# Performance work log

Measured on AMD Instinct MI355X. Metric: run time of the kernel, lower is better.

Reference implementation:

```python
import jax, jax.numpy as jnp
import numpy as np

ATT_HEAD, IN_DIM, OUT_DIM = 8, 768, 96
B, N = 8, 1024
LEAKY_ALPHA = 0.2


def setup_inputs() -> dict:
    key = jax.random.key(0)
    ks = jax.random.split(key, 8)
    feat_in = jax.random.normal(ks[0], (B, N, IN_DIM), dtype=jnp.float32)
    adj = jax.random.randint(ks[1], (B, N, N), 0, 2).astype(jnp.float32)
    # xavier-ish init scales
    W = jax.random.normal(ks[2], (ATT_HEAD, IN_DIM, OUT_DIM), dtype=jnp.float32) * (1.0 / np.sqrt(IN_DIM))
    b = jnp.zeros((OUT_DIM,), dtype=jnp.float32)
    w_src = jax.random.normal(ks[3], (ATT_HEAD, OUT_DIM, 1), dtype=jnp.float32) * (1.0 / np.sqrt(OUT_DIM))
    w_dst = jax.random.normal(ks[4], (ATT_HEAD, OUT_DIM, 1), dtype=jnp.float32) * (1.0 / np.sqrt(OUT_DIM))
    Hw = jax.random.normal(ks[5], (IN_DIM, IN_DIM), dtype=jnp.float32) * (1.0 / np.sqrt(IN_DIM))
    Hb = jnp.zeros((IN_DIM,), dtype=jnp.float32)
    return {"feat_in": feat_in, "adj": adj, "W": W, "b": b,
            "w_src": w_src, "w_dst": w_dst, "Hw": Hw, "Hb": Hb}


def reference(feat_in, adj, W, b, w_src, w_dst, Hw, Hb):
    batch, n, _ = feat_in.shape
    # per-head projection: [B,H,N,O]
    h = jnp.einsum('bni,hio->bhno', feat_in, W)
    t = jnp.tanh(h)
    a_src = jnp.einsum('bhno,hoq->bhnq', t, w_src)[..., 0]  # [B,H,N]
    a_dst = jnp.einsum('bhno,hoq->bhnq', t, w_dst)[..., 0]  # [B,H,N]
    attn = a_src[:, :, :, None] + a_dst[:, :, None, :]       # [B,H,N,N]
    attn = jnp.where(attn >= 0, attn, LEAKY_ALPHA * attn)
    mask = adj[:, None, :, :] == 0                            # 1-adj as bool
    attn = jnp.where(mask, jnp.float32(-999.0), attn)
    attn = jax.nn.softmax(attn, axis=-1)
    feat_out = jnp.einsum('bhnm,bhmo->bhno', attn, h) + b     # [B,H,N,O]
    feat_out = jnp.transpose(feat_out, (0, 2, 1, 3)).reshape(batch, n, -1)
    feat_out = jax.nn.elu(feat_out)
    gate = jax.nn.sigmoid(feat_in @ Hw.T + Hb)
    return gate * feat_out + (1.0 - gate) * feat_in
```

## Files before the change

### kernel.cpp

```cpp
#include <hip/hip_runtime.h>
#include <cstddef>

#define BATCH 8
#define NN 1024
#define IN_DIM 768
#define OUT_DIM 96
#define HEADS 8
#define M_ROWS 8192
#define NCOLS 1536

typedef __attribute__((ext_vector_type(8))) short short8;
typedef __attribute__((ext_vector_type(4))) float f32x4;
typedef __attribute__((ext_vector_type(4))) unsigned short ushort4v;

__device__ __forceinline__ unsigned short f2bf(float x) {
    unsigned int u = __builtin_bit_cast(unsigned int, x);
    u += 0x7fffu + ((u >> 16) & 1u);
    return (unsigned short)(u >> 16);
}
__device__ __forceinline__ float bf2f(unsigned short u) {
    unsigned int v = ((unsigned int)u) << 16;
    return __builtin_bit_cast(float, v);
}
__device__ __forceinline__ float tanh_fast(float x) {
    return 1.f - 2.f / (__expf(2.f * x) + 1.f);
}

__global__ void xb_kernel(const float* __restrict__ x, unsigned short* __restrict__ xb) {
    int idx = blockIdx.x * 256 + threadIdx.x;
    const float4* p = (const float4*)(x + (size_t)idx * 8);
    float4 a = p[0], b = p[1];
    short8 r;
    r[0] = (short)f2bf(a.x); r[1] = (short)f2bf(a.y); r[2] = (short)f2bf(a.z); r[3] = (short)f2bf(a.w);
    r[4] = (short)f2bf(b.x); r[5] = (short)f2bf(b.y); r[6] = (short)f2bf(b.z); r[7] = (short)f2bf(b.w);
    *(short8*)(xb + (size_t)idx * 8) = r;
}

__global__ void pack_w_kernel(const float* __restrict__ W, unsigned short* __restrict__ BT) {
    int idx = blockIdx.x * 256 + threadIdx.x;
    int c = idx / IN_DIM, i = idx % IN_DIM;
    int h = c / OUT_DIM, o = c % OUT_DIM;
    BT[(size_t)c * IN_DIM + i] = f2bf(W[((size_t)h * IN_DIM + i) * OUT_DIM + o]);
}
__global__ void pack_hw_kernel(const float* __restrict__ Hw, unsigned short* __restrict__ BT) {
    int idx = blockIdx.x * 256 + threadIdx.x;
    int c = idx / IN_DIM, i = idx % IN_DIM;
    BT[(size_t)(768 + c) * IN_DIM + i] = f2bf(Hw[(size_t)c * IN_DIM + i]);
}

__global__ void pack_abits_kernel(const float* __restrict__ adj, unsigned int* __restrict__ abits) {
    int idx = blockIdx.x * 256 + threadIdx.x;
    const float4* p = (const float4*)(adj + (size_t)idx * 32);
    unsigned int m = 0;
    #pragma unroll
    for (int q = 0; q < 8; ++q) {
        float4 v = p[q];
        m |= (v.x != 0.f ? 1u : 0u) << (q * 4 + 0);
        m |= (v.y != 0.f ? 1u : 0u) << (q * 4 + 1);
        m |= (v.z != 0.f ? 1u : 0u) << (q * 4 + 2);
        m |= (v.w != 0.f ? 1u : 0u) << (q * 4 + 3);
    }
    abits[idx] = m;
}

__global__ __launch_bounds__(256) void gemm1_kernel(
        const unsigned short* __restrict__ Xb, const unsigned short* __restrict__ BT,
        unsigned short* __restrict__ h_bt, float* __restrict__ glog) {
    __shared__ unsigned short As[128 * 72];
    __shared__ unsigned short Bs[128 * 72];
    int m0 = blockIdx.x * 128;
    int c0 = blockIdx.y * 128;
    int t = threadIdx.x;
    int w = t >> 6, lane = t & 63, l15 = t & 15, quad = lane >> 4;
    f32x4 acc[2][8] = {};
    for (int k0 = 0; k0 < IN_DIM; k0 += 64) {
        __syncthreads();
        #pragma unroll
        for (int q = 0; q < 4; ++q) {
            int f = t + q * 256;
            int r = f >> 3, c8 = (f & 7) * 8;
            *(short8*)(As + r * 72 + c8) = *(const short8*)(Xb + (size_t)(m0 + r) * IN_DIM + k0 + c8);
            *(short8*)(Bs + r * 72 + c8) = *(const short8*)(BT + (size_t)(c0 + r) * IN_DIM + k0 + c8);
        }
        __syncthreads();
        #pragma unroll
        for (int ks = 0; ks < 2; ++ks) {
            short8 af[2], bfr[8];
            #pragma unroll
            for (int mt = 0; mt < 2; ++mt)
                af[mt] = *(const short8*)(As + (w * 32 + mt * 16 + l15) * 72 + ks * 32 + quad * 8);
            #pragma unroll
            for (int nt = 0; nt < 8; ++nt)
                bfr[nt] = *(const short8*)(Bs + (nt * 16 + l15) * 72 + ks * 32 + quad * 8);
            #pragma unroll
            for (int mt = 0; mt < 2; ++mt)
                #pragma unroll
                for (int nt = 0; nt < 8; ++nt)
                    acc[mt][nt] = __builtin_amdgcn_mfma_f32_16x16x32_bf16(af[mt], bfr[nt], acc[mt][nt], 0, 0, 0);
        }
    }
    int b = m0 >> 10;
    #pragma unroll
    for (int mt = 0; mt < 2; ++mt) {
        int rowbase = m0 + w * 32 + mt * 16 + quad * 4;
        int nbase = rowbase & 1023;
        #pragma unroll
        for (int nt = 0; nt < 8; ++nt) {
            int c = c0 + nt * 16 + l15;
            if (c < 768) {
                int hh = c / OUT_DIM, o = c % OUT_DIM;
                ushort4v hb;
                hb[0] = f2bf(acc[mt][nt][0]); hb[1] = f2bf(acc[mt][nt][1]);
                hb[2] = f2bf(acc[mt][nt][2]); hb[3] = f2bf(acc[mt][nt][3]);
                *(ushort4v*)(h_bt + ((size_t)(b * 8 + hh) * OUT_DIM + o) * NN + nbase) = hb;
            } else {
                int cg = c - 768;
                #pragma unroll
                for (int reg = 0; reg < 4; ++reg)
                    glog[(size_t)(rowbase + reg) * 768 + cg] = acc[mt][nt][reg];
            }
        }
    }
}

__global__ __launch_bounds__(256) void a_kernel(const unsigned short* __restrict__ h_bt,
                                                const float* __restrict__ w_src,
                                                const float* __restrict__ w_dst,
                                                float* __restrict__ a_src, float* __restrict__ a_dst) {
    __shared__ unsigned short ht[96 * 72];
    __shared__ float ws_s[96], wd_s[96];
    __shared__ float pps[4][64], ppd[4][64];
    int bh = blockIdx.x >> 4;
    int n0 = (blockIdx.x & 15) * 64;
    int head = bh & 7;
    int t = threadIdx.x;
    if (t < 96) { ws_s[t] = w_src[head * 96 + t]; wd_s[t] = w_dst[head * 96 + t]; }
    for (int f = t; f < 768; f += 256) {
        int row = f >> 3, c8 = (f & 7) * 8;
        *(short8*)(ht + row * 72 + c8) = *(const short8*)(h_bt + ((size_t)bh * 96 + row) * NN + n0 + c8);
    }
    __syncthreads();
    int n = t & 63, part = t >> 6;
    float ps = 0.f, pd = 0.f;
    #pragma unroll
    for (int oo = 0; oo < 24; ++oo) {
        int o = part * 24 + oo;
        float th = tanh_fast(bf2f(ht[o * 72 + n]));
        ps += th * ws_s[o];
        pd += th * wd_s[o];
    }
    pps[part][n] = ps; ppd[part][n] = pd;
    __syncthreads();
    if (t < 64) {
        float s = pps[0][t] + pps[1][t] + pps[2][t] + pps[3][t];
        float d = ppd[0][t] + ppd[1][t] + ppd[2][t] + ppd[3][t];
        a_src[bh * 1024 + n0 + t] = s * 1.44269504f;
        a_dst[bh * 1024 + n0 + t] = d * 1.44269504f;
    }
}

__global__ __launch_bounds__(256) void attn_kernel(
        const unsigned short* __restrict__ h_bt, const unsigned int* __restrict__ abits,
        const float* __restrict__ a_src_g, const float* __restrict__ a_dst_g,
        float* __restrict__ fo_ws) {
    __shared__ __align__(16) unsigned short es[64 * 72];
    __shared__ __align__(16) unsigned short hs[96 * 72];
    __shared__ __align__(16) float adst[1024];
    __shared__ __align__(16) float asrc[64];
    int blk = blockIdx.x;
    int bh = blk >> 4, i0 = (blk & 15) * 64, b = bh >> 3;
    int t = threadIdx.x;
    int w = t >> 6, lane = t & 63, l15 = t & 15, quad = lane >> 4;
    for (int q = 0; q < 4; ++q) adst[q * 256 + t] = a_dst_g[bh * 1024 + q * 256 + t];
    if (t < 64) asrc[t] = a_src_g[bh * 1024 + i0 + t];
    const unsigned short* hhp = h_bt + (size_t)bh * 96 * NN;
    int il = t >> 2, jq = (t & 3) * 16;
    const unsigned int* ab_row = abits + ((size_t)b * NN + i0 + il) * 32;
    short8 hreg[3];
    #pragma unroll
    for (int q = 0; q < 3; ++q) {
        int f = t + q * 256;
        int row = f >> 3, c8 = (f & 7) * 8;
        hreg[q] = *(const short8*)(hhp + (size_t)row * NN + c8);
    }
    unsigned int mword = ab_row[jq >> 5];
    f32x4 acc[7] = {};
    short8 ones = {};
    if (l15 == 0) {
        #pragma unroll
        for (int u = 0; u < 8; ++u) ones[u] = (short)0x3F80;
    }
    __syncthreads();
    float si = asrc[il];
    for (int j0 = 0; j0 < 1024; j0 += 64) {
        #pragma unroll
        for (int q = 0; q < 3; ++q) {
            int f = t + q * 256;
            int row = f >> 3, c8 = (f & 7) * 8;
            *(short8*)(hs + row * 72 + c8) = hreg[q];
        }
        unsigned int m16 = (mword >> (jq & 16)) & 0xFFFFu;
        f32x4 dv[4];
        #pragma unroll
        for (int q = 0; q < 4; ++q) dv[q] = *(const f32x4*)(&adst[j0 + jq + q * 4]);
        float ev[16];
        #pragma unroll
        for (int u = 0; u < 16; ++u) {
            float s = si + dv[u >> 2][u & 3];
            float l = fmaxf(s, 0.2f * s);
            float e = __builtin_amdgcn_exp2f(l);
            ev[u] = ((m16 >> u) & 1u) ? e : 0.f;
        }
        union { unsigned int u[8]; short8 s8[2]; } pk;
        #pragma unroll
        for (int p = 0; p < 8; ++p) {
            unsigned int u0 = __builtin_bit_cast(unsigned int, ev[2 * p]) + 0x8000u;
            unsigned int u1 = __builtin_bit_cast(unsigned int, ev[2 * p + 1]) + 0x8000u;
            pk.u[p] = __builtin_amdgcn_perm(u1, u0, 0x07060302);
        }
        *(short8*)(es + il * 72 + jq) = pk.s8[0];
        *(short8*)(es + il * 72 + jq + 8) = pk.s8[1];
        int jn = j0 + 64;
        if (jn < 1024) {
            #pragma unroll
            for (int q = 0; q < 3; ++q) {
                int f = t + q * 256;
                int row = f >> 3, c8 = (f & 7) * 8;
                hreg[q] = *(const short8*)(hhp + (size_t)row * NN + jn + c8);
            }
            mword = ab_row[(jn + jq) >> 5];
        }
        __syncthreads();
        #pragma unroll
        for (int ks = 0; ks < 2; ++ks) {
            short8 af = *(const short8*)(es + (w * 16 + l15) * 72 + ks * 32 + quad * 8);
            #pragma unroll
            for (int nt = 0; nt < 6; ++nt) {
                short8 bfr = *(const short8*)(hs + (nt * 16 + l15) * 72 + ks * 32 + quad * 8);
                acc[nt] = __builtin_amdgcn_mfma_f32_16x16x32_bf16(af, bfr, acc[nt], 0, 0, 0);
            }
            acc[6] = __builtin_amdgcn_mfma_f32_16x16x32_bf16(af, ones, acc[6], 0, 0, 0);
        }
        __syncthreads();
    }
    int rowq = i0 + w * 16 + quad * 4;
    #pragma unroll
    for (int reg = 0; reg < 4; ++reg) {
        float ssum = __shfl(acc[6][reg], (lane & 48));
        float inv = (ssum > 0.f) ? 1.f / ssum : 0.f;
        float* op = fo_ws + ((size_t)bh * NN + rowq + reg) * OUT_DIM;
        #pragma unroll
        for (int nt = 0; nt < 6; ++nt)
            op[nt * 16 + l15] = acc[nt][reg] * inv;
    }
}

__global__ void epilogue_kernel(const float* __restrict__ fo_ws, const float* __restrict__ glog,
                                const float* __restrict__ feat_in, const float* __restrict__ bias,
                                const float* __restrict__ Hb, float* __restrict__ out) {
    int idx = blockIdx.x * 256 + threadIdx.x;
    int m = idx / 192, c4 = idx % 192;
    int c = c4 * 4;
    int b = m >> 10, n = m & 1023;
    int hh = c / OUT_DIM, o = c % OUT_DIM;
    float4 fo = *(const float4*)(fo_ws + ((size_t)(b * 8 + hh) * NN + n) * OUT_DIM + o);
    float4 gl = *(const float4*)(glog + (size_t)m * 768 + c);
    float4 x  = *(const float4*)(feat_in + (size_t)m * 768 + c);
    float fv[4] = {fo.x, fo.y, fo.z, fo.w};
    float gv[4] = {gl.x, gl.y, gl.z, gl.w};
    float xv[4] = {x.x, x.y, x.z, x.w};
    float r[4];
    #pragma unroll
    for (int u = 0; u < 4; ++u) {
        float v = fv[u] + bias[o + u];
        float e = (v > 0.f) ? v : (__expf(v) - 1.f);
        float g = 1.f / (1.f + __expf(-(gv[u] + Hb[c + u])));
        r[u] = g * e + (1.f - g) * xv[u];
    }
    *(float4*)(out + (size_t)m * 768 + c) = make_float4(r[0], r[1], r[2], r[3]);
}

extern "C" void kernel_launch(void* const* d_in, const int* in_sizes, int n_in,
                              void* d_out, int out_size, void* d_ws, size_t ws_size,
                              hipStream_t stream) {
    const float* feat_in = (const float*)d_in[0];
    const float* adj     = (const float*)d_in[1];
    const float* W       = (const float*)d_in[2];
    const float* bbias   = (const float*)d_in[3];
    const float* w_src   = (const float*)d_in[4];
    const float* w_dst   = (const float*)d_in[5];
    const float* Hw      = (const float*)d_in[6];
    const float* Hb      = (const float*)d_in[7];
    float* out = (float*)d_out;
    char* base = (char*)d_ws;

    unsigned short* Xb    = (unsigned short*)(base);
    unsigned short* BcatT = (unsigned short*)(base + 12582912);
    unsigned short* h_bt  = (unsigned short*)(base + 14942208);
    float* glog  = (float*)(base + 27525120);
    float* a_src = (float*)(base + 52690944);
    float* a_dst = (float*)(base + 52953088);
    float* fo_ws = (float*)(base + 53215232);
    unsigned int* abits = (unsigned int*)(base);

    xb_kernel<<<(M_ROWS * IN_DIM / 8) / 256, 256, 0, stream>>>(feat_in, Xb);
    pack_w_kernel<<<(768 * IN_DIM) / 256, 256, 0, stream>>>(W, BcatT);
    pack_hw_kernel<<<(768 * IN_DIM) / 256, 256, 0, stream>>>(Hw, BcatT);
    gemm1_kernel<<<dim3(M_ROWS / 128, NCOLS / 128), 256, 0, stream>>>(Xb, BcatT, h_bt, glog);
    pack_abits_kernel<<<(BATCH * NN * NN / 32) / 256, 256, 0, stream>>>(adj, abits);
    a_kernel<<<64 * 16, 256, 0, stream>>>(h_bt, w_src, w_dst, a_src, a_dst);
    attn_kernel<<<64 * 16, 256, 0, stream>>>(h_bt, abits, a_src, a_dst, fo_ws);
    epilogue_kernel<<<(M_ROWS * 192) / 256, 256, 0, stream>>>(fo_ws, glog, feat_in, bbias, Hb, out);
}
```

Before: 211.2 us.

## Fuse gating epilogue into attention kernel and use direct-to-LDS loads in GEMM

Removes the separate epilogue kernel: the attention kernel now applies bias, ELU and the sigmoid gate and writes the final output directly. This avoids the write and re-read of the fo_ws intermediate buffer and one launch. Separately, gemm1 now stages tiles with global_load_lds (direct global-to-LDS copies) using an XOR-swizzled unpadded layout instead of register-staged padded copies. The fused epilogue's reads of glog and feat_in are scattered 16-lane 64-byte segments, which may coalesce less well than the old float4 epilogue.

```diff
diff --git a/kernel.cpp b/kernel.cpp
--- a/kernel.cpp
+++ b/kernel.cpp
@@ -12,6 +12,15 @@
 typedef __attribute__((ext_vector_type(8))) short short8;
 typedef __attribute__((ext_vector_type(4))) float f32x4;
 typedef __attribute__((ext_vector_type(4))) unsigned short ushort4v;
+
+typedef __attribute__((address_space(1))) void gvoid_t;
+typedef __attribute__((address_space(3))) void lvoid_t;
+
+__device__ __forceinline__ void gload_lds16(const void* g, void* l) {
+    __builtin_amdgcn_global_load_lds((gvoid_t*)(unsigned long long)g,
+                                     (lvoid_t*)(unsigned int)(unsigned long long)l,
+                                     16, 0, 0);
+}
 
 __device__ __forceinline__ unsigned short f2bf(float x) {
     unsigned int u = __builtin_bit_cast(unsigned int, x);
@@ -66,8 +75,8 @@
 __global__ __launch_bounds__(256) void gemm1_kernel(
         const unsigned short* __restrict__ Xb, const unsigned short* __restrict__ BT,
         unsigned short* __restrict__ h_bt, float* __restrict__ glog) {
-    __shared__ unsigned short As[128 * 72];
-    __shared__ unsigned short Bs[128 * 72];
+    __shared__ __align__(16) unsigned short As[128 * 64];
+    __shared__ __align__(16) unsigned short Bs[128 * 64];
     int m0 = blockIdx.x * 128;
     int c0 = blockIdx.y * 128;
     int t = threadIdx.x;
@@ -76,22 +85,30 @@
     for (int k0 = 0; k0 < IN_DIM; k0 += 64) {
         __syncthreads();
         #pragma unroll
-        for (int q = 0; q < 4; ++q) {
-            int f = t + q * 256;
-            int r = f >> 3, c8 = (f & 7) * 8;
-            *(short8*)(As + r * 72 + c8) = *(const short8*)(Xb + (size_t)(m0 + r) * IN_DIM + k0 + c8);
-            *(short8*)(Bs + r * 72 + c8) = *(const short8*)(BT + (size_t)(c0 + r) * IN_DIM + k0 + c8);
+        for (int cc = 0; cc < 4; ++cc) {
+            int base64 = (w * 4 + cc) * 64;
+            int p = base64 + lane;
+            int r = p >> 3, qs = p & 7;
+            int qb = qs ^ (r & 7);
+            gload_lds16(Xb + (size_t)(m0 + r) * IN_DIM + k0 + qb * 8, As + base64 * 8);
+            gload_lds16(BT + (size_t)(c0 + r) * IN_DIM + k0 + qb * 8, Bs + base64 * 8);
         }
         __syncthreads();
         #pragma unroll
         for (int ks = 0; ks < 2; ++ks) {
             short8 af[2], bfr[8];
             #pragma unroll
-            for (int mt = 0; mt < 2; ++mt)
-                af[mt] = *(const short8*)(As + (w * 32 + mt * 16 + l15) * 72 + ks * 32 + quad * 8);
-            #pragma unroll
-            for (int nt = 0; nt < 8; ++nt)
-                bfr[nt] = *(const short8*)(Bs + (nt * 16 + l15) * 72 + ks * 32 + quad * 8);
+            for (int mt = 0; mt < 2; ++mt) {
+                int r = w * 32 + mt * 16 + l15;
+                int cb = (ks * 4 + quad) ^ (r & 7);
+                af[mt] = *(const short8*)(As + r * 64 + cb * 8);
+            }
+            #pragma unroll
+            for (int nt = 0; nt < 8; ++nt) {
+                int r = nt * 16 + l15;
+                int cb = (ks * 4 + quad) ^ (r & 7);
+                bfr[nt] = *(const short8*)(Bs + r * 64 + cb * 8);
+            }
             #pragma unroll
             for (int mt = 0; mt < 2; ++mt)
                 #pragma unroll
@@ -162,17 +179,21 @@
 __global__ __launch_bounds__(256) void attn_kernel(
         const unsigned short* __restrict__ h_bt, const unsigned int* __restrict__ abits,
         const float* __restrict__ a_src_g, const float* __restrict__ a_dst_g,
-        float* __restrict__ fo_ws) {
+        const float* __restrict__ glog, const float* __restrict__ feat_in,
+        const float* __restrict__ bias, const float* __restrict__ Hb,
+        float* __restrict__ out) {
     __shared__ __align__(16) unsigned short es[64 * 72];
     __shared__ __align__(16) unsigned short hs[96 * 72];
     __shared__ __align__(16) float adst[1024];
     __shared__ __align__(16) float asrc[64];
+    __shared__ float bias_s[96], hb_s[96];
     int blk = blockIdx.x;
-    int bh = blk >> 4, i0 = (blk & 15) * 64, b = bh >> 3;
+    int bh = blk >> 4, i0 = (blk & 15) * 64, b = bh >> 3, hh = bh & 7;
     int t = threadIdx.x;
     int w = t >> 6, lane = t & 63, l15 = t & 15, quad = lane >> 4;
     for (int q = 0; q < 4; ++q) adst[q * 256 + t] = a_dst_g[bh * 1024 + q * 256 + t];
     if (t < 64) asrc[t] = a_src_g[bh * 1024 + i0 + t];
+    if (t >= 64 && t < 160) { bias_s[t - 64] = bias[t - 64]; hb_s[t - 64] = Hb[hh * 96 + t - 64]; }
     const unsigned short* hhp = h_bt + (size_t)bh * 96 * NN;
     int il = t >> 2, jq = (t & 3) * 16;
     const unsigned int* ab_row = abits + ((size_t)b * NN + i0 + il) * 32;
@@ -248,36 +269,19 @@
     for (int reg = 0; reg < 4; ++reg) {
         float ssum = __shfl(acc[6][reg], (lane & 48));
         float inv = (ssum > 0.f) ? 1.f / ssum : 0.f;
-        float* op = fo_ws + ((size_t)bh * NN + rowq + reg) * OUT_DIM;
-        #pragma unroll
-        for (int nt = 0; nt < 6; ++nt)
-            op[nt * 16 + l15] = acc[nt][reg] * inv;
-    }
-}
-
-__global__ void epilogue_kernel(const float* __restrict__ fo_ws, const float* __restrict__ glog,
-                                const float* __restrict__ feat_in, const float* __restrict__ bias,
-                                const float* __restrict__ Hb, float* __restrict__ out) {
-    int idx = blockIdx.x * 256 + threadIdx.x;
-    int m = idx / 192, c4 = idx % 192;
-    int c = c4 * 4;
-    int b = m >> 10, n = m & 1023;
-    int hh = c / OUT_DIM, o = c % OUT_DIM;
-    float4 fo = *(const float4*)(fo_ws + ((size_t)(b * 8 + hh) * NN + n) * OUT_DIM + o);
-    float4 gl = *(const float4*)(glog + (size_t)m * 768 + c);
-    float4 x  = *(const float4*)(feat_in + (size_t)m * 768 + c);
-    float fv[4] = {fo.x, fo.y, fo.z, fo.w};
-    float gv[4] = {gl.x, gl.y, gl.z, gl.w};
-    float xv[4] = {x.x, x.y, x.z, x.w};
-    float r[4];
-    #pragma unroll
-    for (int u = 0; u < 4; ++u) {
-        float v = fv[u] + bias[o + u];
-        float e = (v > 0.f) ? v : (__expf(v) - 1.f);
-        float g = 1.f / (1.f + __expf(-(gv[u] + Hb[c + u])));
-        r[u] = g * e + (1.f - g) * xv[u];
-    }
-    *(float4*)(out + (size_t)m * 768 + c) = make_float4(r[0], r[1], r[2], r[3]);
+        int n = rowq + reg;
+        size_t mrow = ((size_t)b * NN + n) * 768 + hh * 96;
+        #pragma unroll
+        for (int nt = 0; nt < 6; ++nt) {
+            int cl = nt * 16 + l15;
+            float fo = acc[nt][reg] * inv + bias_s[cl];
+            float e = (fo > 0.f) ? fo : (__expf(fo) - 1.f);
+            float z = glog[mrow + cl] + hb_s[cl];
+            float g = 1.f / (1.f + __expf(-z));
+            float x = feat_in[mrow + cl];
+            out[mrow + cl] = g * e + (1.f - g) * x;
+        }
+    }
 }
 
 extern "C" void kernel_launch(void* const* d_in, const int* in_sizes, int n_in,
@@ -300,7 +304,6 @@
     float* glog  = (float*)(base + 27525120);
     float* a_src = (float*)(base + 52690944);
     float* a_dst = (float*)(base + 52953088);
-    float* fo_ws = (float*)(base + 53215232);
     unsigned int* abits = (unsigned int*)(base);
 
     xb_kernel<<<(M_ROWS * IN_DIM / 8) / 256, 256, 0, stream>>>(feat_in, Xb);
@@ -309,6 +312,5 @@
     gemm1_kernel<<<dim3(M_ROWS / 128, NCOLS / 128), 256, 0, stream>>>(Xb, BcatT, h_bt, glog);
     pack_abits_kernel<<<(BATCH * NN * NN / 32) / 256, 256, 0, stream>>>(adj, abits);
     a_kernel<<<64 * 16, 256, 0, stream>>>(h_bt, w_src, w_dst, a_src, a_dst);
-    attn_kernel<<<64 * 16, 256, 0, stream>>>(h_bt, abits, a_src, a_dst, fo_ws);
-    epilogue_kernel<<<(M_ROWS * 192) / 256, 256, 0, stream>>>(fo_ws, glog, feat_in, bbias, Hb, out);
-}
+    attn_kernel<<<64 * 16, 256, 0, stream>>>(h_bt, abits, a_src, a_dst, glog, feat_in, bbias, Hb, out);
+}
```

Measured after the change: 195.9 us. 1.08x faster.
